# Optimization experiments

Hardware: AMD Instinct MI355X
Metric: run time of the kernel (lower is better)

The kernel has to match this reference:

```python
import jax, jax.numpy as jnp
import numpy as np

N_NODES = 100000
N_EDGES = 3200000
IN_DIM, HID_DIM, N_CLASS = 64, 32, 20


def setup_inputs() -> dict:
    key = jax.random.key(0)
    k1, k2, k3, k4, k5, k6 = jax.random.split(key, 6)
    x = jax.random.normal(k1, (N_NODES, IN_DIM), dtype=jnp.float32)
    edge_index = jax.random.randint(k2, (2, N_EDGES), 0, N_NODES, dtype=jnp.int64)
    W1 = jax.random.normal(k3, (IN_DIM, HID_DIM), dtype=jnp.float32) / np.sqrt(IN_DIM)
    b1 = jnp.zeros((HID_DIM,), dtype=jnp.float32)
    Wout = jax.random.normal(k4, (HID_DIM, N_CLASS), dtype=jnp.float32) / np.sqrt(HID_DIM)
    bout = jnp.zeros((N_CLASS,), dtype=jnp.float32)
    return {"x": x, "edge_index": edge_index, "W1": W1, "b1": b1, "Wout": Wout, "bout": bout}


def gcn_conv(x, edge_index, W, b):
    # PyG GCNConv defaults: add self-loops, symmetric deg^{-1/2} normalization.
    n = x.shape[0]
    loop = jnp.arange(n, dtype=edge_index.dtype)
    row = jnp.concatenate([edge_index[0], loop])  # source
    col = jnp.concatenate([edge_index[1], loop])  # target
    deg = jax.ops.segment_sum(jnp.ones_like(col, dtype=x.dtype), col, num_segments=n)
    dis = jnp.where(deg > 0, deg ** -0.5, 0.0)
    norm = dis[row] * dis[col]  # [E+N]
    xw = x @ W  # [N, HID]
    msg = norm[:, None] * xw[row]  # [E+N, HID]
    agg = jax.ops.segment_sum(msg, col, num_segments=n)
    return agg + b


def reference(x, edge_index, W1, b1, Wout, bout):
    h = gcn_conv(x, edge_index, W1, b1)
    emb = jax.nn.relu(h)
    return emb @ Wout + bout
```

## Files before the change

kernel.cpp:

```cpp
#include <hip/hip_runtime.h>
#include <hip/hip_fp16.h>
#include <math.h>

#define N_NODES 100000
#define N_EDGES 3200000
#define IN_DIM 64
#define HID_DIM 32
#define N_CLASS 20

#define BKT_BITS 6
#define BKT_W    64
#define NBKT     1563
#define CAP_BKT  2560
#define HALF_W   32
#define CAP_D    1536
#define CHUNK    8192
#define NBLK_E   ((N_EDGES + CHUNK - 1) / CHUNK)

__global__ void k_detect(const int* __restrict__ ei32, int* __restrict__ flag,
                         int* __restrict__ gcursor) {
    __shared__ int any;
    if (threadIdx.x == 0) any = 0;
    __syncthreads();
    int nz = 0;
    for (int k = threadIdx.x; k < 4096; k += blockDim.x)
        if (ei32[2 * k + 1] != 0) nz = 1;
    if (nz) atomicOr(&any, 1);
    for (int i = threadIdx.x; i < NBKT; i += blockDim.x) gcursor[i] = i * CAP_BKT;
    __syncthreads();
    if (threadIdx.x == 0) *flag = any ? 0 : 1;
}

__device__ __forceinline__ int get_idx(const int* __restrict__ ei32, int wide, int pos) {
    return wide ? ei32[2 * (long long)pos] : ei32[pos];
}

__global__ void kC_scatter(const int* __restrict__ ei32, const int* __restrict__ flag,
                           int* __restrict__ gcursor, unsigned int* __restrict__ pk) {
    __shared__ int lh[NBKT];
    __shared__ int lgb[NBKT];
    __shared__ int lrt[NBKT];
    int wide = *flag;
    for (int i = threadIdx.x; i < NBKT; i += blockDim.x) { lh[i] = 0; lrt[i] = 0; }
    __syncthreads();
    int base = blockIdx.x * CHUNK;
    int src[8], dst[8];
#pragma unroll
    for (int k = 0; k < 8; ++k) {
        int e = base + k * 1024 + threadIdx.x;
        if (e < N_EDGES) {
            src[k] = get_idx(ei32, wide, e);
            dst[k] = get_idx(ei32, wide, N_EDGES + e);
            atomicAdd(&lh[dst[k] >> BKT_BITS], 1);
        } else dst[k] = -1;
    }
    __syncthreads();
    for (int b = threadIdx.x; b < NBKT; b += blockDim.x)
        if (lh[b]) lgb[b] = atomicAdd(&gcursor[b], lh[b]);
    __syncthreads();
#pragma unroll
    for (int k = 0; k < 8; ++k) {
        if (dst[k] >= 0) {
            int b = dst[k] >> BKT_BITS;
            int r = atomicAdd(&lrt[b], 1);
            int pos = lgb[b] + r;
            if (pos < (b + 1) * CAP_BKT)
                pk[pos] = ((unsigned)src[k] << BKT_BITS) | (unsigned)(dst[k] & (BKT_W - 1));
        }
    }
}

__global__ void kC1_deg(const unsigned int* __restrict__ pk, const int* __restrict__ gcursor,
                        float* __restrict__ dis) {
    __shared__ int lcnt[BKT_W];
    int b = blockIdx.x;
    int gb = b * CAP_BKT;
    int bsz = min(gcursor[b] - gb, CAP_BKT);
    if (threadIdx.x < BKT_W) lcnt[threadIdx.x] = 0;
    __syncthreads();
    for (int i = threadIdx.x; i < bsz; i += blockDim.x)
        atomicAdd(&lcnt[pk[gb + i] & (BKT_W - 1)], 1);
    __syncthreads();
    int node = b * BKT_W + threadIdx.x;
    if (threadIdx.x < BKT_W && node < N_NODES)
        dis[node] = rsqrtf((float)(lcnt[threadIdx.x] + 1));
}

__global__ void k_xw(const float* __restrict__ x, const float* __restrict__ W1,
                     const float* __restrict__ dis, __half* __restrict__ xw16) {
    __shared__ float sW[IN_DIM * HID_DIM];
    for (int i = threadIdx.x; i < IN_DIM * HID_DIM; i += blockDim.x) sW[i] = W1[i];
    __syncthreads();
    int tid = blockIdx.x * blockDim.x + threadIdx.x;
    int node = tid >> 3;
    int q = tid & 7;
    if (node >= N_NODES) return;
    const float4* xr = reinterpret_cast<const float4*>(x + (size_t)node * IN_DIM);
    float4 a = make_float4(0.f, 0.f, 0.f, 0.f);
#pragma unroll
    for (int k4 = 0; k4 < IN_DIM / 4; ++k4) {
        float4 xv = xr[k4];
        const float4 w0 = *reinterpret_cast<const float4*>(&sW[(k4 * 4 + 0) * HID_DIM + q * 4]);
        const float4 w1 = *reinterpret_cast<const float4*>(&sW[(k4 * 4 + 1) * HID_DIM + q * 4]);
        const float4 w2 = *reinterpret_cast<const float4*>(&sW[(k4 * 4 + 2) * HID_DIM + q * 4]);
        const float4 w3 = *reinterpret_cast<const float4*>(&sW[(k4 * 4 + 3) * HID_DIM + q * 4]);
        a.x += xv.x * w0.x + xv.y * w1.x + xv.z * w2.x + xv.w * w3.x;
        a.y += xv.x * w0.y + xv.y * w1.y + xv.z * w2.y + xv.w * w3.y;
        a.z += xv.x * w0.z + xv.y * w1.z + xv.z * w2.z + xv.w * w3.z;
        a.w += xv.x * w0.w + xv.y * w1.w + xv.z * w2.w + xv.w * w3.w;
    }
    float d = dis[node];
    union { __half2 h2[2]; uint2 u; } cvt;
    cvt.h2[0] = __floats2half2_rn(a.x * d, a.y * d);
    cvt.h2[1] = __floats2half2_rn(a.z * d, a.w * d);
    *reinterpret_cast<uint2*>(xw16 + (size_t)node * HID_DIM + q * 4) = cvt.u;
}

__global__ void kD_gather(const unsigned int* __restrict__ pk, const int* __restrict__ gcursor,
                          const float* __restrict__ dis, const __half* __restrict__ xw16,
                          const float* __restrict__ b1, const float* __restrict__ Wout,
                          const float* __restrict__ bout, float* __restrict__ out) {
    __shared__ int   ssrc[CAP_D];
    __shared__ int   lcnt[HALF_W], lstart[HALF_W], lrt[HALF_W];
    __shared__ int   stot;
    __shared__ float sW[HID_DIM * N_CLASS];
    __shared__ float sb1[HID_DIM];
    __shared__ float sbo[N_CLASS];
    for (int i = threadIdx.x; i < HID_DIM * N_CLASS; i += blockDim.x) sW[i] = Wout[i];
    if (threadIdx.x < HID_DIM) sb1[threadIdx.x] = b1[threadIdx.x];
    if (threadIdx.x < N_CLASS) sbo[threadIdx.x] = bout[threadIdx.x];
    if (threadIdx.x < HALF_W) { lcnt[threadIdx.x] = 0; lrt[threadIdx.x] = 0; }
    int B = blockIdx.x;
    int b = B >> 1, h = B & 1;
    int gb = b * CAP_BKT;
    int bsz = min(gcursor[b] - gb, CAP_BKT);
    __syncthreads();

    for (int i = threadIdx.x; i < bsz; i += blockDim.x) {
        int ld = (int)(pk[gb + i] & (BKT_W - 1));
        if ((ld >> 5) == h) atomicAdd(&lcnt[ld & (HALF_W - 1)], 1);
    }
    __syncthreads();
    if (threadIdx.x == 0) {
        int acc = 0;
        for (int n = 0; n < HALF_W; ++n) { lstart[n] = acc; acc += lcnt[n]; }
        stot = acc;
    }
    __syncthreads();
    bool fits = (stot <= CAP_D);
    if (fits) {
        for (int i = threadIdx.x; i < bsz; i += blockDim.x) {
            unsigned v = pk[gb + i];
            int ld = (int)(v & (BKT_W - 1));
            if ((ld >> 5) == h) {
                int r = atomicAdd(&lrt[ld & (HALF_W - 1)], 1);
                ssrc[lstart[ld & (HALF_W - 1)] + r] = (int)(v >> BKT_BITS);
            }
        }
    }
    __syncthreads();

    int grp = threadIdx.x >> 3, part = threadIdx.x & 7;
    int ln = grp;
    int node = b * BKT_W + h * HALF_W + ln;
    if (node >= N_NODES) return;
    union U { unsigned u; __half2 hh; };
    float4 acc = make_float4(0.f, 0.f, 0.f, 0.f);
    if (fits) {
        int s0 = lstart[ln], s1 = s0 + lcnt[ln];
#pragma unroll 4
        for (int e = s0; e < s1; ++e) {
            int src = ssrc[e];
            uint2 u = *reinterpret_cast<const uint2*>(xw16 + (size_t)src * HID_DIM + part * 4);
            U a0; a0.u = u.x; U a1; a1.u = u.y;
            float2 f0 = __half22float2(a0.hh);
            float2 f1 = __half22float2(a1.hh);
            acc.x += f0.x; acc.y += f0.y; acc.z += f1.x; acc.w += f1.y;
        }
    } else {
        int want = h * HALF_W + ln;
        for (int i = 0; i < bsz; ++i) {
            unsigned v = pk[gb + i];
            if ((int)(v & (BKT_W - 1)) == want) {
                int src = (int)(v >> BKT_BITS);
                uint2 u = *reinterpret_cast<const uint2*>(xw16 + (size_t)src * HID_DIM + part * 4);
                U a0; a0.u = u.x; U a1; a1.u = u.y;
                float2 f0 = __half22float2(a0.hh);
                float2 f1 = __half22float2(a1.hh);
                acc.x += f0.x; acc.y += f0.y; acc.z += f1.x; acc.w += f1.y;
            }
        }
    }
    {
        uint2 u = *reinterpret_cast<const uint2*>(xw16 + (size_t)node * HID_DIM + part * 4);
        U a0; a0.u = u.x; U a1; a1.u = u.y;
        float2 f0 = __half22float2(a0.hh);
        float2 f1 = __half22float2(a1.hh);
        acc.x += f0.x; acc.y += f0.y; acc.z += f1.x; acc.w += f1.y;
    }
    float dc = dis[node];
    float e0 = fmaxf(dc * acc.x + sb1[part * 4 + 0], 0.f);
    float e1 = fmaxf(dc * acc.y + sb1[part * 4 + 1], 0.f);
    float e2 = fmaxf(dc * acc.z + sb1[part * 4 + 2], 0.f);
    float e3 = fmaxf(dc * acc.w + sb1[part * 4 + 3], 0.f);
    float o[N_CLASS];
#pragma unroll
    for (int cl = 0; cl < N_CLASS; ++cl) {
        o[cl] = e0 * sW[(part * 4 + 0) * N_CLASS + cl]
              + e1 * sW[(part * 4 + 1) * N_CLASS + cl]
              + e2 * sW[(part * 4 + 2) * N_CLASS + cl]
              + e3 * sW[(part * 4 + 3) * N_CLASS + cl];
    }
#pragma unroll
    for (int m = 1; m < 8; m <<= 1) {
#pragma unroll
        for (int cl = 0; cl < N_CLASS; ++cl) o[cl] += __shfl_xor(o[cl], m, 64);
    }
    if (part < 5) {
        float4 w = make_float4(o[part * 4 + 0] + sbo[part * 4 + 0],
                               o[part * 4 + 1] + sbo[part * 4 + 1],
                               o[part * 4 + 2] + sbo[part * 4 + 2],
                               o[part * 4 + 3] + sbo[part * 4 + 3]);
        *reinterpret_cast<float4*>(out + (size_t)node * N_CLASS + part * 4) = w;
    }
}

extern "C" void kernel_launch(void* const* d_in, const int* in_sizes, int n_in,
                              void* d_out, int out_size, void* d_ws, size_t ws_size,
                              hipStream_t stream) {
    const float* x    = (const float*)d_in[0];
    const int*   ei32 = (const int*)d_in[1];
    const float* W1   = (const float*)d_in[2];
    const float* b1   = (const float*)d_in[3];
    const float* Wout = (const float*)d_in[4];
    const float* bout = (const float*)d_in[5];
    float* out = (float*)d_out;

    __half*       xw16    = (__half*)d_ws;
    unsigned int* pk      = (unsigned int*)((char*)d_ws + (size_t)N_NODES * HID_DIM * 2);
    int*          gcursor = (int*)(pk + (size_t)NBKT * CAP_BKT);
    float*        dis     = (float*)(gcursor + NBKT);
    int*          flag    = (int*)(dis + N_NODES);

    k_detect<<<1, 256, 0, stream>>>(ei32, flag, gcursor);
    kC_scatter<<<NBLK_E, 1024, 0, stream>>>(ei32, flag, gcursor, pk);
    kC1_deg<<<NBKT, 256, 0, stream>>>(pk, gcursor, dis);
    k_xw<<<(N_NODES * 8 + 255) / 256, 256, 0, stream>>>(x, W1, dis, xw16);
    kD_gather<<<2 * NBKT, 256, 0, stream>>>(pk, gcursor, dis, xw16, b1, Wout, bout, out);
}
```

Before: 110.8 us.

## Retune scatter blocks and cache bucket entries in registers in gather

The scatter kernel now runs 256-thread blocks over 4096-edge chunks, with 16 edges per thread and launch bounds set. The gather kernel loads its bucket entries into registers once and reuses them for both the count pass and the fill pass. It replaces the serial single-thread prefix sum with a wavefront shuffle scan, and batches the neighbour row loads 8 at a time to raise memory-level parallelism. In exchange, smaller chunks mean more global cursor atomics, and register pressure is higher.

```diff
diff --git a/kernel.cpp b/kernel.cpp
--- a/kernel.cpp
+++ b/kernel.cpp
@@ -14,8 +14,10 @@
 #define CAP_BKT  2560
 #define HALF_W   32
 #define CAP_D    1536
-#define CHUNK    8192
+#define CHUNK    4096
+#define EPT      16
 #define NBLK_E   ((N_EDGES + CHUNK - 1) / CHUNK)
+#define ENT_R    (CAP_BKT / 256)
 
 __global__ void k_detect(const int* __restrict__ ei32, int* __restrict__ flag,
                          int* __restrict__ gcursor) {
@@ -35,8 +37,9 @@
     return wide ? ei32[2 * (long long)pos] : ei32[pos];
 }
 
-__global__ void kC_scatter(const int* __restrict__ ei32, const int* __restrict__ flag,
-                           int* __restrict__ gcursor, unsigned int* __restrict__ pk) {
+__global__ void __launch_bounds__(256, 8)
+kC_scatter(const int* __restrict__ ei32, const int* __restrict__ flag,
+           int* __restrict__ gcursor, unsigned int* __restrict__ pk) {
     __shared__ int lh[NBKT];
     __shared__ int lgb[NBKT];
     __shared__ int lrt[NBKT];
@@ -44,10 +47,10 @@
     for (int i = threadIdx.x; i < NBKT; i += blockDim.x) { lh[i] = 0; lrt[i] = 0; }
     __syncthreads();
     int base = blockIdx.x * CHUNK;
-    int src[8], dst[8];
-#pragma unroll
-    for (int k = 0; k < 8; ++k) {
-        int e = base + k * 1024 + threadIdx.x;
+    int src[EPT], dst[EPT];
+#pragma unroll
+    for (int k = 0; k < EPT; ++k) {
+        int e = base + k * 256 + threadIdx.x;
         if (e < N_EDGES) {
             src[k] = get_idx(ei32, wide, e);
             dst[k] = get_idx(ei32, wide, N_EDGES + e);
@@ -59,7 +62,7 @@
         if (lh[b]) lgb[b] = atomicAdd(&gcursor[b], lh[b]);
     __syncthreads();
 #pragma unroll
-    for (int k = 0; k < 8; ++k) {
+    for (int k = 0; k < EPT; ++k) {
         if (dst[k] >= 0) {
             int b = dst[k] >> BKT_BITS;
             int r = atomicAdd(&lrt[b], 1);
@@ -116,10 +119,19 @@
     *reinterpret_cast<uint2*>(xw16 + (size_t)node * HID_DIM + q * 4) = cvt.u;
 }
 
-__global__ void kD_gather(const unsigned int* __restrict__ pk, const int* __restrict__ gcursor,
-                          const float* __restrict__ dis, const __half* __restrict__ xw16,
-                          const float* __restrict__ b1, const float* __restrict__ Wout,
-                          const float* __restrict__ bout, float* __restrict__ out) {
+__device__ __forceinline__ void acc_row(float4& acc, uint2 u) {
+    union U { unsigned u; __half2 hh; };
+    U a0; a0.u = u.x; U a1; a1.u = u.y;
+    float2 f0 = __half22float2(a0.hh);
+    float2 f1 = __half22float2(a1.hh);
+    acc.x += f0.x; acc.y += f0.y; acc.z += f1.x; acc.w += f1.y;
+}
+
+__global__ void __launch_bounds__(256, 8)
+kD_gather(const unsigned int* __restrict__ pk, const int* __restrict__ gcursor,
+          const float* __restrict__ dis, const __half* __restrict__ xw16,
+          const float* __restrict__ b1, const float* __restrict__ Wout,
+          const float* __restrict__ bout, float* __restrict__ out) {
     __shared__ int   ssrc[CAP_D];
     __shared__ int   lcnt[HALF_W], lstart[HALF_W], lrt[HALF_W];
     __shared__ int   stot;
@@ -136,25 +148,42 @@
     int bsz = min(gcursor[b] - gb, CAP_BKT);
     __syncthreads();
 
-    for (int i = threadIdx.x; i < bsz; i += blockDim.x) {
-        int ld = (int)(pk[gb + i] & (BKT_W - 1));
-        if ((ld >> 5) == h) atomicAdd(&lcnt[ld & (HALF_W - 1)], 1);
-    }
-    __syncthreads();
-    if (threadIdx.x == 0) {
-        int acc = 0;
-        for (int n = 0; n < HALF_W; ++n) { lstart[n] = acc; acc += lcnt[n]; }
-        stot = acc;
+    unsigned ents[ENT_R];
+#pragma unroll
+    for (int i = 0; i < ENT_R; ++i) {
+        int idx = i * 256 + (int)threadIdx.x;
+        ents[i] = (idx < bsz) ? pk[gb + idx] : 0xFFFFFFFFu;
+    }
+#pragma unroll
+    for (int i = 0; i < ENT_R; ++i) {
+        if (ents[i] != 0xFFFFFFFFu) {
+            int ld = (int)(ents[i] & (BKT_W - 1));
+            if ((ld >> 5) == h) atomicAdd(&lcnt[ld & (HALF_W - 1)], 1);
+        }
+    }
+    __syncthreads();
+    if (threadIdx.x < HALF_W) {
+        int v = lcnt[threadIdx.x];
+        int s = v;
+#pragma unroll
+        for (int d = 1; d < HALF_W; d <<= 1) {
+            int t = __shfl_up(s, d, HALF_W);
+            if ((int)(threadIdx.x & (HALF_W - 1)) >= d) s += t;
+        }
+        lstart[threadIdx.x] = s - v;
+        if (threadIdx.x == HALF_W - 1) stot = s;
     }
     __syncthreads();
     bool fits = (stot <= CAP_D);
     if (fits) {
-        for (int i = threadIdx.x; i < bsz; i += blockDim.x) {
-            unsigned v = pk[gb + i];
-            int ld = (int)(v & (BKT_W - 1));
-            if ((ld >> 5) == h) {
-                int r = atomicAdd(&lrt[ld & (HALF_W - 1)], 1);
-                ssrc[lstart[ld & (HALF_W - 1)] + r] = (int)(v >> BKT_BITS);
+#pragma unroll
+        for (int i = 0; i < ENT_R; ++i) {
+            if (ents[i] != 0xFFFFFFFFu) {
+                int ld = (int)(ents[i] & (BKT_W - 1));
+                if ((ld >> 5) == h) {
+                    int r = atomicAdd(&lrt[ld & (HALF_W - 1)], 1);
+                    ssrc[lstart[ld & (HALF_W - 1)] + r] = (int)(ents[i] >> BKT_BITS);
+                }
             }
         }
     }
@@ -164,41 +193,38 @@
     int ln = grp;
     int node = b * BKT_W + h * HALF_W + ln;
     if (node >= N_NODES) return;
-    union U { unsigned u; __half2 hh; };
+
     float4 acc = make_float4(0.f, 0.f, 0.f, 0.f);
+    acc_row(acc, *reinterpret_cast<const uint2*>(xw16 + (size_t)node * HID_DIM + part * 4));
+    float dc = dis[node];
+
     if (fits) {
-        int s0 = lstart[ln], s1 = s0 + lcnt[ln];
-#pragma unroll 4
-        for (int e = s0; e < s1; ++e) {
+        int s0 = lstart[ln], cnt = lcnt[ln];
+        int e = s0, end = s0 + cnt;
+        while (e + 8 <= end) {
+            int srcs[8];
+#pragma unroll
+            for (int j = 0; j < 8; ++j) srcs[j] = ssrc[e + j];
+            uint2 us[8];
+#pragma unroll
+            for (int j = 0; j < 8; ++j)
+                us[j] = *reinterpret_cast<const uint2*>(xw16 + (size_t)srcs[j] * HID_DIM + part * 4);
+#pragma unroll
+            for (int j = 0; j < 8; ++j) acc_row(acc, us[j]);
+            e += 8;
+        }
+        for (; e < end; ++e) {
             int src = ssrc[e];
-            uint2 u = *reinterpret_cast<const uint2*>(xw16 + (size_t)src * HID_DIM + part * 4);
-            U a0; a0.u = u.x; U a1; a1.u = u.y;
-            float2 f0 = __half22float2(a0.hh);
-            float2 f1 = __half22float2(a1.hh);
-            acc.x += f0.x; acc.y += f0.y; acc.z += f1.x; acc.w += f1.y;
+            acc_row(acc, *reinterpret_cast<const uint2*>(xw16 + (size_t)src * HID_DIM + part * 4));
         }
     } else {
         int want = h * HALF_W + ln;
         for (int i = 0; i < bsz; ++i) {
             unsigned v = pk[gb + i];
-            if ((int)(v & (BKT_W - 1)) == want) {
-                int src = (int)(v >> BKT_BITS);
-                uint2 u = *reinterpret_cast<const uint2*>(xw16 + (size_t)src * HID_DIM + part * 4);
-                U a0; a0.u = u.x; U a1; a1.u = u.y;
-                float2 f0 = __half22float2(a0.hh);
-                float2 f1 = __half22float2(a1.hh);
-                acc.x += f0.x; acc.y += f0.y; acc.z += f1.x; acc.w += f1.y;
-            }
-        }
-    }
-    {
-        uint2 u = *reinterpret_cast<const uint2*>(xw16 + (size_t)node * HID_DIM + part * 4);
-        U a0; a0.u = u.x; U a1; a1.u = u.y;
-        float2 f0 = __half22float2(a0.hh);
-        float2 f1 = __half22float2(a1.hh);
-        acc.x += f0.x; acc.y += f0.y; acc.z += f1.x; acc.w += f1.y;
-    }
-    float dc = dis[node];
+            if ((int)(v & (BKT_W - 1)) == want)
+                acc_row(acc, *reinterpret_cast<const uint2*>(xw16 + (size_t)(v >> BKT_BITS) * HID_DIM + part * 4));
+        }
+    }
     float e0 = fmaxf(dc * acc.x + sb1[part * 4 + 0], 0.f);
     float e1 = fmaxf(dc * acc.y + sb1[part * 4 + 1], 0.f);
     float e2 = fmaxf(dc * acc.z + sb1[part * 4 + 2], 0.f);
@@ -243,7 +269,7 @@
     int*          flag    = (int*)(dis + N_NODES);
 
     k_detect<<<1, 256, 0, stream>>>(ei32, flag, gcursor);
-    kC_scatter<<<NBLK_E, 1024, 0, stream>>>(ei32, flag, gcursor, pk);
+    kC_scatter<<<NBLK_E, 256, 0, stream>>>(ei32, flag, gcursor, pk);
     kC1_deg<<<NBKT, 256, 0, stream>>>(pk, gcursor, dis);
     k_xw<<<(N_NODES * 8 + 255) / 256, 256, 0, stream>>>(x, W1, dis, xw16);
     kD_gather<<<2 * NBKT, 256, 0, stream>>>(pk, gcursor, dis, xw16, b1, Wout, bout, out);
```

New measurement: 137.5 us. +24.1%, slower.
